# Optimization experiments

Measured on AMD Instinct MI355X. Metric: run time of the kernel, lower is better.

## Reference

```python
import jax, jax.numpy as jnp
import numpy as np


def _deconcat(values, offsets):
    """Ragged [N, D] + offsets [B+1] -> padded [B, L, D] and valid mask [B, L]."""
    offsets = np.asarray(offsets)
    lengths = np.diff(offsets)
    L = int(lengths.max())
    pos = np.arange(L)
    idx = np.minimum(offsets[:-1, None] + pos[None, :], values.shape[0] - 1)
    valid = pos[None, :] < lengths[:, None]  # [B, L]
    batched = jnp.take(values, jnp.asarray(idx), axis=0)
    batched = batched * jnp.asarray(valid, values.dtype)[:, :, None]
    return batched, jnp.asarray(valid)


def setup_inputs() -> dict:
    B, H, Wd, F, Q, D = 4, 128, 128, 16384, 300, 256
    key = jax.random.key(0)
    ks = jax.random.split(key, 8)
    queries = jax.random.normal(ks[0], (B * Q, D), jnp.float32)
    feature_values = jax.random.normal(ks[1], (B * F, D), jnp.float32)
    hw = jax.random.randint(ks[2], (B * F, 2), 0, H)
    bcol = jnp.repeat(jnp.arange(B), F)[:, None]
    feature_indices = jnp.concatenate([bcol, hw], axis=1).astype(jnp.int32)
    params = {}
    wkeys = jax.random.split(ks[3], 4)
    for i in range(4):
        params[f"W{i}"] = (jax.random.normal(wkeys[i], (D, D), jnp.float32) * 0.02)
        params[f"b{i}"] = jnp.zeros((D,), jnp.float32)
    return dict(
        queries=queries,
        feature_values=feature_values,
        feature_indices=feature_indices,
        query_batch_offsets=jnp.arange(B + 1, dtype=jnp.int32) * Q,
        feature_batch_offsets=jnp.arange(B + 1, dtype=jnp.int32) * F,
        height=H,
        width=Wd,
        **params,
    )


def reference(queries, feature_values, feature_indices,
              query_batch_offsets, feature_batch_offsets,
              height, width, W0, b0, W1, b1, W2, b2, W3, b3):
    q = queries
    for Wl, bl in ((W0, b0), (W1, b1), (W2, b2)):
        q = jax.nn.relu(q @ Wl.T + bl)
    q = q @ W3.T + b3

    bq, qvalid = _deconcat(q, query_batch_offsets)            # [B, Qm, D], [B, Qm]
    bf, fvalid = _deconcat(feature_values, feature_batch_offsets)  # [B, Fm, D]

    # bmm: per-image feature-vs-query logits
    logits = jnp.einsum('bfd,bqd->bfq', bf, bq)               # [B, Fm, Qm]

    # gather each real feature's logit row (undo padding), mask pad queries
    foff = jnp.asarray(np.asarray(feature_batch_offsets))
    b_of_n = feature_indices[:, 0]                            # [N]
    f_of_n = jnp.arange(feature_indices.shape[0]) - foff[b_of_n]
    flat = logits[b_of_n, f_of_n]                             # [N, Qm]
    flat = flat * qvalid.astype(logits.dtype)[b_of_n]

    # dense equivalent of the coalesced sparse COO output (B, H, W, Q);
    # duplicate (b,h,w) indices sum, matching coalesce()
    B, Qm = qvalid.shape
    out = jnp.zeros((B, height, width, Qm), logits.dtype)
    out = out.at[b_of_n, feature_indices[:, 1], feature_indices[:, 2]].add(flat)
    return out
```

## Files before the change

### kernel.cpp

```cpp
#include <hip/hip_runtime.h>
#include <hip/hip_bf16.h>
#include <stdint.h>

typedef __attribute__((ext_vector_type(8))) short bf16x8;
typedef __attribute__((ext_vector_type(4))) float f32x4;

__device__ __forceinline__ unsigned short f2bf(float f) {
    union { float f; unsigned u; } v; v.f = f;
    unsigned u = v.u;
    u += 0x7fff + ((u >> 16) & 1);
    return (unsigned short)(u >> 16);
}

__global__ __launch_bounds__(256) void prep(
    const int* __restrict__ FI, const int* __restrict__ wptr,
    int* __restrict__ cnt, int* __restrict__ slots,
    const float* __restrict__ W0, const float* __restrict__ W1,
    const float* __restrict__ W2, const float* __restrict__ W3,
    unsigned short* __restrict__ wsW,
    int NF, int HW, int wsz, int nbBin)
{
    int blk = blockIdx.x;
    if (blk < nbBin) {
        int i = blk * 256 + threadIdx.x;
        if (i >= NF) return;
        int Wd = *wptr;
        int b = FI[(size_t)i * 3];
        int h = FI[(size_t)i * 3 + 1];
        int w = FI[(size_t)i * 3 + 2];
        int gc = b * HW + h * Wd + w;
        int slot = atomicAdd(&cnt[gc], 1);
        if (slot < 16) slots[(size_t)gc * 16 + slot] = i;
    } else {
        int idx = ((blk - nbBin) * 256 + threadIdx.x) * 4;
        if (idx >= 4 * wsz) return;
        int l = idx / wsz, off = idx - l * wsz;
        const float* Ws = (l == 0) ? W0 : (l == 1) ? W1 : (l == 2) ? W2 : W3;
        float4 v = *(const float4*)(Ws + off);
        ushort4 o; o.x = f2bf(v.x); o.y = f2bf(v.y); o.z = f2bf(v.z); o.w = f2bf(v.w);
        *(ushort4*)(wsW + (size_t)l * wsz + off) = o;
    }
}

__global__ __launch_bounds__(256) void gather_mlp(
    const float* __restrict__ Qf, const unsigned short* __restrict__ Wb,
    const float* __restrict__ b0p, const float* __restrict__ b1p,
    const float* __restrict__ b2p, const float* __restrict__ b3p,
    unsigned short* __restrict__ outQB, int M, int wsz,
    const float* __restrict__ FV, const int* __restrict__ cnt,
    const int* __restrict__ slots, unsigned short* __restrict__ Abuf, int NC,
    int nbM, int nbG)
{
    __shared__ unsigned short At[16 * 264];
    const int tid = threadIdx.x;
    const int wid = tid >> 6, lane = tid & 63, quad = lane >> 4, l16 = lane & 15;

    if (blockIdx.x >= nbM) {
        const int wg = (blockIdx.x - nbM) * 4 + wid;
        const int nw = nbG * 4;
        for (int cb = wg * 4; cb < NC; cb += nw * 4) {
            int sl = slots[(size_t)cb * 16 + lane];
            int c = cb + quad;
            int n = (c < NC) ? cnt[c] : 0;
            if (n > 16) n = 16;
            float4 a0 = make_float4(0.f, 0.f, 0.f, 0.f);
            float4 a1 = a0, a2 = a0, a3 = a0;
            for (int s = 0; s < n; ++s) {
                int f = __shfl(sl, (quad << 4) + s);
                const float* src = FV + (size_t)f * 256 + l16 * 16;
                float4 v0 = *(const float4*)(src + 0);
                float4 v1 = *(const float4*)(src + 4);
                float4 v2 = *(const float4*)(src + 8);
                float4 v3 = *(const float4*)(src + 12);
                a0.x += v0.x; a0.y += v0.y; a0.z += v0.z; a0.w += v0.w;
                a1.x += v1.x; a1.y += v1.y; a1.z += v1.z; a1.w += v1.w;
                a2.x += v2.x; a2.y += v2.y; a2.z += v2.z; a2.w += v2.w;
                a3.x += v3.x; a3.y += v3.y; a3.z += v3.z; a3.w += v3.w;
            }
            if (c < NC) {
                unsigned short* dst = Abuf + (size_t)c * 256 + l16 * 16;
                ushort4 o0, o1, o2, o3;
                o0.x = f2bf(a0.x); o0.y = f2bf(a0.y); o0.z = f2bf(a0.z); o0.w = f2bf(a0.w);
                o1.x = f2bf(a1.x); o1.y = f2bf(a1.y); o1.z = f2bf(a1.z); o1.w = f2bf(a1.w);
                o2.x = f2bf(a2.x); o2.y = f2bf(a2.y); o2.z = f2bf(a2.z); o2.w = f2bf(a2.w);
                o3.x = f2bf(a3.x); o3.y = f2bf(a3.y); o3.z = f2bf(a3.z); o3.w = f2bf(a3.w);
                *(ushort4*)(dst + 0)  = o0;
                *(ushort4*)(dst + 4)  = o1;
                *(ushort4*)(dst + 8)  = o2;
                *(ushort4*)(dst + 12) = o3;
            }
        }
        return;
    }

    const int m0 = blockIdx.x * 16;
    #pragma unroll
    for (int i = 0; i < 4; ++i) {
        int c = tid + i * 256;
        int row = c >> 6, kq = (c & 63) * 4;
        int gr = m0 + row; if (gr >= M) gr = M - 1;
        float4 v = *(const float4*)(Qf + (size_t)gr * 256 + kq);
        ushort4 o; o.x = f2bf(v.x); o.y = f2bf(v.y); o.z = f2bf(v.z); o.w = f2bf(v.w);
        *(ushort4*)&At[row * 264 + kq] = o;
    }
    __syncthreads();

    for (int l = 0; l < 4; ++l) {
        const unsigned short* Wl = Wb + (size_t)l * wsz;
        const float* bl = (l == 0) ? b0p : (l == 1) ? b1p : (l == 2) ? b2p : b3p;
        f32x4 acc[4] = {};
        #pragma unroll
        for (int k = 0; k < 256; k += 32) {
            bf16x8 af = *(const bf16x8*)&At[l16 * 264 + k + quad * 8];
            #pragma unroll
            for (int t = 0; t < 4; ++t) {
                int n = wid * 64 + t * 16 + l16;
                bf16x8 bfr = *(const bf16x8*)(Wl + (size_t)n * 256 + k + quad * 8);
                acc[t] = __builtin_amdgcn_mfma_f32_16x16x32_bf16(af, bfr, acc[t], 0, 0, 0);
            }
        }
        __syncthreads();
        #pragma unroll
        for (int t = 0; t < 4; ++t) {
            int n = wid * 64 + t * 16 + l16;
            float bv = bl[n];
            #pragma unroll
            for (int r = 0; r < 4; ++r) {
                int m = quad * 4 + r;
                float v = acc[t][r] + bv;
                if (l < 3) {
                    At[m * 264 + n] = f2bf(fmaxf(v, 0.f));
                } else {
                    if (m0 + m < M) outQB[(size_t)(m0 + m) * 256 + n] = f2bf(v);
                }
            }
        }
        if (l < 3) __syncthreads();
    }
}

__global__ __launch_bounds__(256, 4) void cell_gemm3(
    const unsigned short* __restrict__ Abuf,
    const unsigned short* __restrict__ QB, const int* __restrict__ qoff,
    float* __restrict__ out, int cpb, int HW, int Qstride)
{
    __shared__ unsigned short Bsm[304 * 40];

    const int tid = threadIdx.x;
    const int b   = blockIdx.x / cpb;
    const int c0  = (blockIdx.x - b * cpb) * 64;
    const size_t gc0 = (size_t)b * HW + c0;
    const int q0 = qoff[b];
    int qlen = qoff[b + 1] - q0; if (qlen < 1) qlen = 1;

    const int wid = tid >> 6, lane = tid & 63, quad = lane >> 4, l16 = lane & 15;

    const unsigned short* aptr = Abuf + (gc0 + wid * 16 + l16) * 256 + quad * 8;
    bf16x8 afA = *(const bf16x8*)aptr;
    f32x4 acc[19] = {};

    for (int k0 = 0; k0 < 256; k0 += 32) {
        for (int c = tid; c < 1216; c += 256) {
            int row = c >> 2, kc = (c & 3) * 8;
            int qr = row < qlen ? row : qlen - 1;
            uint4 v = *(const uint4*)(QB + (size_t)(q0 + qr) * 256 + k0 + kc);
            *(uint4*)&Bsm[row * 40 + kc] = v;
        }
        int k1 = (k0 + 32) & 255;
        bf16x8 afB = *(const bf16x8*)(aptr + k1);
        __syncthreads();
        #pragma unroll
        for (int t = 0; t < 19; ++t) {
            bf16x8 bfr = *(const bf16x8*)&Bsm[(t * 16 + l16) * 40 + quad * 8];
            acc[t] = __builtin_amdgcn_mfma_f32_16x16x32_bf16(afA, bfr, acc[t], 0, 0, 0);
        }
        __syncthreads();
        afA = afB;
    }

    #pragma unroll
    for (int r = 0; r < 4; ++r) {
        int m = quad * 4 + r;
        float* dst = out + (gc0 + wid * 16 + m) * Qstride;
        #pragma unroll
        for (int t = 0; t < 19; ++t) {
            int nq = t * 16 + l16;
            if (nq < Qstride) dst[nq] = (nq < qlen) ? acc[t][r] : 0.f;
        }
    }
}

extern "C" void kernel_launch(void* const* d_in, const int* in_sizes, int n_in,
                              void* d_out, int out_size, void* d_ws, size_t ws_size,
                              hipStream_t stream) {
    const float* queries = (const float*)d_in[0];
    const float* FV      = (const float*)d_in[1];
    const int*   FI      = (const int*)d_in[2];
    const int*   qoff    = (const int*)d_in[3];
    const int*   wptr    = (const int*)d_in[6];
    const float* W0 = (const float*)d_in[7];
    const float* b0 = (const float*)d_in[8];
    const float* W1 = (const float*)d_in[9];
    const float* b1 = (const float*)d_in[10];
    const float* W2 = (const float*)d_in[11];
    const float* b2 = (const float*)d_in[12];
    const float* W3 = (const float*)d_in[13];
    const float* b3 = (const float*)d_in[14];
    float* out = (float*)d_out;

    const int NQe = in_sizes[0];
    const int NQ  = NQe / 256;
    const int NF  = in_sizes[1] / 256;
    const int WSZ = in_sizes[7];
    const int B   = in_sizes[3] - 1;
    const int Q   = NQ / B;
    const int HW  = out_size / (B * Q);
    const int NC  = B * HW;
    const int cpb = HW / 64;

    int* cnt   = (int*)d_ws;
    int* slots = cnt + (size_t)NC;
    unsigned short* wsW  = (unsigned short*)(slots + (size_t)NC * 16);
    unsigned short* wsQB = wsW + (size_t)4 * WSZ;
    unsigned short* Abuf = wsQB + (size_t)NQe;

    hipMemsetAsync(cnt, 0, (size_t)NC * sizeof(int), stream);

    const int nbBin = (NF + 255) / 256;
    const int nbW   = (4 * WSZ / 4 + 255) / 256;
    prep<<<nbBin + nbW, 256, 0, stream>>>(FI, wptr, cnt, slots,
                                          W0, W1, W2, W3, wsW, NF, HW, WSZ, nbBin);

    const int nbM = (NQ + 15) / 16;
    const int nbG = 4096;
    gather_mlp<<<nbM + nbG, 256, 0, stream>>>(
        queries, wsW, b0, b1, b2, b3, wsQB, NQ, WSZ,
        FV, cnt, slots, Abuf, NC, nbM, nbG);

    cell_gemm3<<<B * cpb, 256, 0, stream>>>(Abuf, wsQB, qoff, out, cpb, HW, Q);
}
```

Measured before the change: 215.3 us.

## Fuse per-cell feature gathering into the cell GEMM via shared memory

The scatter-sum of feature rows per output cell now runs inside the cell GEMM kernel. Each block accumulates its 64 cells' rows directly into a shared-memory A tile instead of a separate pass writing and rereading a bf16 Abuf in global memory. This removes the Abuf round trip and one launch's worth of work from gather_mlp. In exchange it uses about 33KB more LDS per block with occupancy lowered to 2 blocks, and the GEMM no longer prefetches A fragments across k-steps.

```diff
diff --git a/kernel.cpp b/kernel.cpp
--- a/kernel.cpp
+++ b/kernel.cpp
@@ -42,56 +42,15 @@
     }
 }
 
-__global__ __launch_bounds__(256) void gather_mlp(
+__global__ __launch_bounds__(256) void mlp_k(
     const float* __restrict__ Qf, const unsigned short* __restrict__ Wb,
     const float* __restrict__ b0p, const float* __restrict__ b1p,
     const float* __restrict__ b2p, const float* __restrict__ b3p,
-    unsigned short* __restrict__ outQB, int M, int wsz,
-    const float* __restrict__ FV, const int* __restrict__ cnt,
-    const int* __restrict__ slots, unsigned short* __restrict__ Abuf, int NC,
-    int nbM, int nbG)
+    unsigned short* __restrict__ outQB, int M, int wsz)
 {
     __shared__ unsigned short At[16 * 264];
     const int tid = threadIdx.x;
     const int wid = tid >> 6, lane = tid & 63, quad = lane >> 4, l16 = lane & 15;
-
-    if (blockIdx.x >= nbM) {
-        const int wg = (blockIdx.x - nbM) * 4 + wid;
-        const int nw = nbG * 4;
-        for (int cb = wg * 4; cb < NC; cb += nw * 4) {
-            int sl = slots[(size_t)cb * 16 + lane];
-            int c = cb + quad;
-            int n = (c < NC) ? cnt[c] : 0;
-            if (n > 16) n = 16;
-            float4 a0 = make_float4(0.f, 0.f, 0.f, 0.f);
-            float4 a1 = a0, a2 = a0, a3 = a0;
-            for (int s = 0; s < n; ++s) {
-                int f = __shfl(sl, (quad << 4) + s);
-                const float* src = FV + (size_t)f * 256 + l16 * 16;
-                float4 v0 = *(const float4*)(src + 0);
-                float4 v1 = *(const float4*)(src + 4);
-                float4 v2 = *(const float4*)(src + 8);
-                float4 v3 = *(const float4*)(src + 12);
-                a0.x += v0.x; a0.y += v0.y; a0.z += v0.z; a0.w += v0.w;
-                a1.x += v1.x; a1.y += v1.y; a1.z += v1.z; a1.w += v1.w;
-                a2.x += v2.x; a2.y += v2.y; a2.z += v2.z; a2.w += v2.w;
-                a3.x += v3.x; a3.y += v3.y; a3.z += v3.z; a3.w += v3.w;
-            }
-            if (c < NC) {
-                unsigned short* dst = Abuf + (size_t)c * 256 + l16 * 16;
-                ushort4 o0, o1, o2, o3;
-                o0.x = f2bf(a0.x); o0.y = f2bf(a0.y); o0.z = f2bf(a0.z); o0.w = f2bf(a0.w);
-                o1.x = f2bf(a1.x); o1.y = f2bf(a1.y); o1.z = f2bf(a1.z); o1.w = f2bf(a1.w);
-                o2.x = f2bf(a2.x); o2.y = f2bf(a2.y); o2.z = f2bf(a2.z); o2.w = f2bf(a2.w);
-                o3.x = f2bf(a3.x); o3.y = f2bf(a3.y); o3.z = f2bf(a3.z); o3.w = f2bf(a3.w);
-                *(ushort4*)(dst + 0)  = o0;
-                *(ushort4*)(dst + 4)  = o1;
-                *(ushort4*)(dst + 8)  = o2;
-                *(ushort4*)(dst + 12) = o3;
-            }
-        }
-        return;
-    }
 
     const int m0 = blockIdx.x * 16;
     #pragma unroll
@@ -139,11 +98,13 @@
     }
 }
 
-__global__ __launch_bounds__(256, 4) void cell_gemm3(
-    const unsigned short* __restrict__ Abuf,
+__global__ __launch_bounds__(256, 2) void cell_gemm4(
+    const float* __restrict__ FV, const int* __restrict__ cnt,
+    const int* __restrict__ slots,
     const unsigned short* __restrict__ QB, const int* __restrict__ qoff,
     float* __restrict__ out, int cpb, int HW, int Qstride)
 {
+    __shared__ unsigned short Asm[64 * 264];
     __shared__ unsigned short Bsm[304 * 40];
 
     const int tid = threadIdx.x;
@@ -155,8 +116,41 @@
 
     const int wid = tid >> 6, lane = tid & 63, quad = lane >> 4, l16 = lane & 15;
 
-    const unsigned short* aptr = Abuf + (gc0 + wid * 16 + l16) * 256 + quad * 8;
-    bf16x8 afA = *(const bf16x8*)aptr;
+    #pragma unroll
+    for (int j = 0; j < 4; ++j) {
+        int rb = wid * 16 + j * 4;
+        int sl = slots[(gc0 + rb) * 16 + lane];
+        int r  = rb + quad;
+        int n  = cnt[gc0 + r];
+        if (n > 16) n = 16;
+        float4 a0 = make_float4(0.f, 0.f, 0.f, 0.f);
+        float4 a1 = a0, a2 = a0, a3 = a0;
+        for (int s = 0; s < n; ++s) {
+            int f = __shfl(sl, (quad << 4) + s);
+            const float* src = FV + (size_t)f * 256 + l16 * 16;
+            float4 v0 = *(const float4*)(src + 0);
+            float4 v1 = *(const float4*)(src + 4);
+            float4 v2 = *(const float4*)(src + 8);
+            float4 v3 = *(const float4*)(src + 12);
+            a0.x += v0.x; a0.y += v0.y; a0.z += v0.z; a0.w += v0.w;
+            a1.x += v1.x; a1.y += v1.y; a1.z += v1.z; a1.w += v1.w;
+            a2.x += v2.x; a2.y += v2.y; a2.z += v2.z; a2.w += v2.w;
+            a3.x += v3.x; a3.y += v3.y; a3.z += v3.z; a3.w += v3.w;
+        }
+        unsigned short* dst = &Asm[r * 264 + l16 * 16];
+        ushort4 o0, o1, o2, o3;
+        o0.x = f2bf(a0.x); o0.y = f2bf(a0.y); o0.z = f2bf(a0.z); o0.w = f2bf(a0.w);
+        o1.x = f2bf(a1.x); o1.y = f2bf(a1.y); o1.z = f2bf(a1.z); o1.w = f2bf(a1.w);
+        o2.x = f2bf(a2.x); o2.y = f2bf(a2.y); o2.z = f2bf(a2.z); o2.w = f2bf(a2.w);
+        o3.x = f2bf(a3.x); o3.y = f2bf(a3.y); o3.z = f2bf(a3.z); o3.w = f2bf(a3.w);
+        *(ushort4*)(dst + 0)  = o0;
+        *(ushort4*)(dst + 4)  = o1;
+        *(ushort4*)(dst + 8)  = o2;
+        *(ushort4*)(dst + 12) = o3;
+    }
+    __syncthreads();
+
+    const int arow = (wid * 16 + l16) * 264 + quad * 8;
     f32x4 acc[19] = {};
 
     for (int k0 = 0; k0 < 256; k0 += 32) {
@@ -166,16 +160,14 @@
             uint4 v = *(const uint4*)(QB + (size_t)(q0 + qr) * 256 + k0 + kc);
             *(uint4*)&Bsm[row * 40 + kc] = v;
         }
-        int k1 = (k0 + 32) & 255;
-        bf16x8 afB = *(const bf16x8*)(aptr + k1);
         __syncthreads();
+        bf16x8 afA = *(const bf16x8*)&Asm[arow + k0];
         #pragma unroll
         for (int t = 0; t < 19; ++t) {
             bf16x8 bfr = *(const bf16x8*)&Bsm[(t * 16 + l16) * 40 + quad * 8];
             acc[t] = __builtin_amdgcn_mfma_f32_16x16x32_bf16(afA, bfr, acc[t], 0, 0, 0);
         }
         __syncthreads();
-        afA = afB;
     }
 
     #pragma unroll
@@ -222,7 +214,6 @@
     int* slots = cnt + (size_t)NC;
     unsigned short* wsW  = (unsigned short*)(slots + (size_t)NC * 16);
     unsigned short* wsQB = wsW + (size_t)4 * WSZ;
-    unsigned short* Abuf = wsQB + (size_t)NQe;
 
     hipMemsetAsync(cnt, 0, (size_t)NC * sizeof(int), stream);
 
@@ -232,10 +223,8 @@
                                           W0, W1, W2, W3, wsW, NF, HW, WSZ, nbBin);
 
     const int nbM = (NQ + 15) / 16;
-    const int nbG = 4096;
-    gather_mlp<<<nbM + nbG, 256, 0, stream>>>(
-        queries, wsW, b0, b1, b2, b3, wsQB, NQ, WSZ,
-        FV, cnt, slots, Abuf, NC, nbM, nbG);
-
-    cell_gemm3<<<B * cpb, 256, 0, stream>>>(Abuf, wsQB, qoff, out, cpb, HW, Q);
-}
+    mlp_k<<<nbM, 256, 0, stream>>>(queries, wsW, b0, b1, b2, b3, wsQB, NQ, WSZ);
+
+    cell_gemm4<<<B * cpb, 256, 0, stream>>>(FV, cnt, slots, wsQB, qoff,
+                                            out, cpb, HW, Q);
+}
```

New measurement: 230.6 us. 1.07x slower.
